# Kernel tuning notes

Hardware: AMD Instinct MI355X
Metric: run time of the kernel (lower is better)

Reference implementation:

```python
import jax, jax.numpy as jnp
import numpy as np

B, S, E = 2, 2048, 2048
H = 16              # num value heads
D = E // H // 2     # = 64, half head dim (Q/K head dim)
LAMBDA_INIT = 0.8 - 0.6 * float(np.exp(-0.3 * 12))
NORM_EPS = 1e-5


def setup_inputs() -> dict:
    key = jax.random.key(0)
    ks = jax.random.split(key, 10)
    std = 0.02
    x = jax.random.normal(ks[0], (B, S, E), jnp.float32)
    Wq = jax.random.normal(ks[1], (E, E), jnp.float32) * std
    Wk = jax.random.normal(ks[2], (E, E), jnp.float32) * std
    Wv = jax.random.normal(ks[3], (E, E), jnp.float32) * std
    Wo = jax.random.normal(ks[4], (E, E), jnp.float32) * std
    lambda_q1 = jax.random.normal(ks[5], (D,), jnp.float32) * 0.1
    lambda_q2 = jax.random.normal(ks[6], (D,), jnp.float32) * 0.1
    lambda_k1 = jax.random.normal(ks[7], (D,), jnp.float32) * 0.1
    lambda_k2 = jax.random.normal(ks[8], (D,), jnp.float32) * 0.1
    norm_w = jnp.ones((2 * D,), jnp.float32)
    # standard RoPE angle table: (S, D//2)
    inv_freq = 1.0 / (10000.0 ** (np.arange(0, D, 2, dtype=np.float32) / D))
    ang = np.outer(np.arange(S, dtype=np.float32), inv_freq)
    freqs_cos = jnp.asarray(np.cos(ang), jnp.float32)
    freqs_sin = jnp.asarray(np.sin(ang), jnp.float32)
    return {"x": x, "Wq": Wq, "Wk": Wk, "Wv": Wv, "Wo": Wo,
            "lambda_q1": lambda_q1, "lambda_q2": lambda_q2,
            "lambda_k1": lambda_k1, "lambda_k2": lambda_k2,
            "norm_w": norm_w, "freqs_cos": freqs_cos, "freqs_sin": freqs_sin,
            "start_pos": 0}


def _rope(t, cos, sin):
    # t: (B, S, nh, D); complex rotation over pairs along last dim
    tr = t.reshape(*t.shape[:-1], -1, 2)
    tre, tim = tr[..., 0], tr[..., 1]
    c = cos[None, :, None, :]
    s = sin[None, :, None, :]
    out_re = tre * c - tim * s
    out_im = tre * s + tim * c
    return jnp.stack([out_re, out_im], axis=-1).reshape(t.shape)


def reference(x, Wq, Wk, Wv, Wo, lambda_q1, lambda_q2, lambda_k1, lambda_k2,
              norm_w, freqs_cos, freqs_sin, start_pos):
    bsz, tgt_len, _ = x.shape
    scaling = D ** (-0.5)
    q = (x @ Wq.T).reshape(bsz, tgt_len, 2 * H, D)
    k = (x @ Wk.T).reshape(bsz, tgt_len, 2 * H, D)
    v = (x @ Wv.T).reshape(bsz, tgt_len, H, 2 * D)
    q = _rope(q, freqs_cos, freqs_sin)
    k = _rope(k, freqs_cos, freqs_sin)
    q = (q * scaling).transpose(0, 2, 1, 3)      # (B, 2H, S, D)
    keys = k.transpose(0, 2, 1, 3)               # (B, 2H, S, D)
    values = v.transpose(0, 2, 1, 3)             # (B, H, S, 2D)
    scores = jnp.einsum('bhsd,bhtd->bhst', q, keys)
    causal = jnp.where(jnp.arange(tgt_len)[None, :] > jnp.arange(tgt_len)[:, None],
                       jnp.float32(-jnp.inf), jnp.float32(0.0))
    scores = scores + causal
    attn = jax.nn.softmax(scores.astype(jnp.float32), axis=-1)
    lam1 = jnp.exp(jnp.sum(lambda_q1 * lambda_k1))
    lam2 = jnp.exp(jnp.sum(lambda_q2 * lambda_k2))
    lambda_full = lam1 - lam2 + LAMBDA_INIT
    attn = attn.reshape(bsz, H, 2, tgt_len, tgt_len)
    attn_diff = attn[:, :, 0] - lambda_full * attn[:, :, 1]   # (B, H, S, S)
    ctx = jnp.einsum('bhst,bhtd->bhsd', attn_diff, values)    # (B, H, S, 2D)
    # per-head RMSNorm over 2D channel dim
    ctx = ctx * jax.lax.rsqrt(jnp.mean(ctx * ctx, axis=-1, keepdims=True) + NORM_EPS)
    ctx = ctx * norm_w
    ctx = ctx.transpose(0, 2, 1, 3).reshape(bsz, tgt_len, H * 2 * D)
    return ctx @ Wo.T
```

## Files before the change

kernel.cpp:

```cpp
#include <hip/hip_runtime.h>
#include <hip/hip_bf16.h>
#include <stdint.h>

typedef __hip_bfloat16 bf16;
typedef __attribute__((ext_vector_type(8))) short short8;
typedef __attribute__((ext_vector_type(4))) short s4v;
typedef __attribute__((ext_vector_type(4))) float floatx4;

#define MFMA16(a, b, c) __builtin_amdgcn_mfma_f32_16x16x32_bf16((a), (b), (c), 0, 0, 0)
#define LAMBDA_INIT_F 0.7836057665f
#define FENCE() asm volatile("" ::: "memory")

__device__ __forceinline__ void async16(const void* g, void* l) {
    __builtin_amdgcn_global_load_lds(
        (const __attribute__((address_space(1))) void*)g,
        (__attribute__((address_space(3))) void*)(uintptr_t)l,
        16, 0, 0);
}

__device__ __forceinline__ float loadf(const void* p, size_t idx, int isbf) {
    if (isbf) return __bfloat162float(((const bf16*)p)[idx]);
    return ((const float*)p)[idx];
}

__global__ void detect_dtype(const unsigned short* __restrict__ x, int* __restrict__ flag) {
    const int t = threadIdx.x;
    const unsigned short u = x[2 * t];
    const int e = (u >> 7) & 0xFF;
    int sane = (e >= 110 && e <= 130) ? 1 : 0;
#pragma unroll
    for (int m = 32; m > 0; m >>= 1) sane += __shfl_xor(sane, m);
    if (t == 0) flag[0] = (sane >= 32) ? 1 : 0;
}

__device__ __forceinline__ void conv_body(const void* src, bf16* dst, int boff,
                                          int isbf) {
    const int i = (boff * 256 + threadIdx.x) * 8;
    if (isbf) {
        *(short8*)(dst + i) = *(const short8*)((const bf16*)src + i);
    } else {
        const float* f = (const float*)src + i;
        short8 r;
#pragma unroll
        for (int j = 0; j < 8; ++j) {
            bf16 h = __float2bfloat16(f[j]);
            r[j] = __builtin_bit_cast(short, h);
        }
        *(short8*)(dst + i) = r;
    }
}

__global__ __launch_bounds__(256) void convert_all(const void* __restrict__ x,
                                                   const void* __restrict__ Wq,
                                                   const void* __restrict__ Wk,
                                                   const void* __restrict__ Wv,
                                                   bf16* __restrict__ xb,
                                                   bf16* __restrict__ wq,
                                                   bf16* __restrict__ wk,
                                                   bf16* __restrict__ wv,
                                                   const int* __restrict__ flag) {
    const int bid  = blockIdx.x;
    const int isbf = flag[0];
    if (bid < 4096)      { conv_body(x, xb, bid, isbf); }
    else if (bid < 6144) { if (isbf) return; conv_body(Wq, wq, bid - 4096, 0); }
    else if (bid < 8192) { if (isbf) return; conv_body(Wk, wk, bid - 6144, 0); }
    else                 { if (isbf) return; conv_body(Wv, wv, bid - 8192, 0); }
}

__global__ __launch_bounds__(256) void to_bf16(const void* __restrict__ src,
                                               bf16* __restrict__ dst, int n,
                                               const int* __restrict__ flag,
                                               int skip_if_bf16) {
    if (skip_if_bf16 && flag[0]) return;
    const int i = (blockIdx.x * 256 + threadIdx.x) * 8;
    if (i >= n) return;
    conv_body(src, dst, blockIdx.x, flag[0]);
}

template <int BNT>
__device__ __forceinline__ void gemm_core256(const bf16* __restrict__ A,
                                             const bf16* __restrict__ B,
                                             void* __restrict__ C,
                                             int N, int bm, int bnl,
                                             const int* __restrict__ flag,
                                             const void* __restrict__ fcos,
                                             const void* __restrict__ fsin,
                                             int mode, char* lds) {
    constexpr int K    = 2048;
    constexpr int NT   = 64;
    constexpr int ASZ  = 16384;
    constexpr int BSZ  = BNT * 64;
    constexpr int SLOT = ASZ + BSZ;
    constexpr int F    = (BNT == 256) ? 8 : 4;
    constexpr int FH   = F / 2;
    constexpr int BCH  = BNT / 128;

    const int tid  = threadIdx.x;
    const int lane = tid & 63;
    const int quad = lane >> 4;
    const int l16  = lane & 15;
    const int w    = tid >> 6;
    const int wr   = (BNT == 256) ? (w >> 2) : (w >> 1);
    const int wc   = (BNT == 256) ? (w & 3) : (w & 1);

    const int c0 = tid, c1 = tid + 512;
    const int r0 = c0 >> 2, r1 = c1 >> 2;
    const int kc0 = (c0 & 3) ^ (((r0 >> 3) & 1) << 1);
    const int kc1 = (c1 & 3) ^ (((r1 >> 3) & 1) << 1);
    const bf16* Asrc0 = A + (size_t)(bm * 256 + r0) * K + kc0 * 8;
    const bf16* Asrc1 = A + (size_t)(bm * 256 + r1) * K + kc1 * 8;
    const bf16* Bsrc0 = B + (size_t)(bnl * BNT + r0) * K + kc0 * 8;
    const bf16* Bsrc1 = B + (size_t)(bnl * BNT + r1) * K + kc1 * 8;
    const int dA0 = c0 * 16, dA1 = c1 * 16;
    const int dB0 = ASZ + c0 * 16, dB1 = ASZ + c1 * 16;

    const int swz = (quad * 16) ^ ((l16 & 8) << 2);
    int offA[8], offB[4];
#pragma unroll
    for (int f = 0; f < F; ++f) offA[f] = (wr * (F * 16) + f * 16 + l16) * 64 + swz;
#pragma unroll
    for (int g = 0; g < 4; ++g) offB[g] = ASZ + (wc * 64 + g * 16 + l16) * 64 + swz;

    floatx4 acc[F][4];
#pragma unroll
    for (int f = 0; f < F; ++f)
#pragma unroll
        for (int g = 0; g < 4; ++g)
#pragma unroll
            for (int r = 0; r < 4; ++r) acc[f][g][r] = 0.0f;

#pragma unroll
    for (int ts = 0; ts < 2; ++ts) {
        char* slot = lds + ts * SLOT;
        async16(Asrc0 + ts * 32, slot + dA0);
        async16(Asrc1 + ts * 32, slot + dA1);
        async16(Bsrc0 + ts * 32, slot + dB0);
        if constexpr (BCH == 2) async16(Bsrc1 + ts * 32, slot + dB1);
    }
    if constexpr (BNT == 256) asm volatile("s_waitcnt vmcnt(4)" ::: "memory");
    else                      asm volatile("s_waitcnt vmcnt(3)" ::: "memory");
    __builtin_amdgcn_s_barrier();
    FENCE();

#pragma unroll 4
    for (int t = 0; t < NT; ++t) {
        char* slot  = lds + (t & 3) * SLOT;
        const int ts = t + 2;
        char* wslot = lds + (ts & 3) * SLOT;

        short8 af[FH], bfv[4];
#pragma unroll
        for (int f = 0; f < FH; ++f) af[f] = *(const short8*)(slot + offA[f]);
#pragma unroll
        for (int g = 0; g < 4; ++g) bfv[g] = *(const short8*)(slot + offB[g]);
        if (ts < NT) {
            async16(Asrc0 + (size_t)ts * 32, wslot + dA0);
            async16(Asrc1 + (size_t)ts * 32, wslot + dA1);
        }
        FENCE();
        __builtin_amdgcn_s_barrier();
        FENCE();
        __builtin_amdgcn_s_setprio(1);
#pragma unroll
        for (int f = 0; f < FH; ++f)
#pragma unroll
            for (int g = 0; g < 4; ++g)
                acc[f][g] = MFMA16(af[f], bfv[g], acc[f][g]);
        __builtin_amdgcn_s_setprio(0);

        short8 af2[FH];
#pragma unroll
        for (int f = 0; f < FH; ++f) af2[f] = *(const short8*)(slot + offA[FH + f]);
        if (ts < NT) {
            async16(Bsrc0 + (size_t)ts * 32, wslot + dB0);
            if constexpr (BCH == 2) async16(Bsrc1 + (size_t)ts * 32, wslot + dB1);
            if constexpr (BNT == 256) asm volatile("s_waitcnt vmcnt(4)" ::: "memory");
            else                      asm volatile("s_waitcnt vmcnt(3)" ::: "memory");
        } else {
            asm volatile("s_waitcnt vmcnt(0)" ::: "memory");
        }
        __builtin_amdgcn_s_barrier();
        FENCE();
        __builtin_amdgcn_s_setprio(1);
#pragma unroll
        for (int f = 0; f < FH; ++f)
#pragma unroll
            for (int g = 0; g < 4; ++g)
                acc[FH + f][g] = MFMA16(af2[f], bfv[g], acc[FH + f][g]);
        __builtin_amdgcn_s_setprio(0);
    }

    const int isbf  = flag[0];
    const int mbase = bm * 256 + wr * (F * 16);
    const int nbase = bnl * BNT + wc * 64;
    if (mode == 3) {
#pragma unroll
        for (int f = 0; f < F; ++f)
#pragma unroll
            for (int g = 0; g < 4; ++g) {
                const int n  = nbase + g * 16 + l16;
                const int m0 = mbase + f * 16 + quad * 4;
                const int bb2 = m0 >> 11;
                const int s0 = m0 & 2047;
                s4v pk;
#pragma unroll
                for (int r = 0; r < 4; ++r) {
                    bf16 hv = __float2bfloat16(acc[f][g][r]);
                    pk[r] = __builtin_bit_cast(short, hv);
                }
                *(s4v*)((bf16*)C + ((size_t)(bb2 * 2048 + n)) * 2048 + s0) = pk;
            }
    } else if (mode == 1 || mode == 2) {
        const float qs = (mode == 1) ? 0.125f : 1.0f;
#pragma unroll
        for (int f = 0; f < F; ++f)
#pragma unroll
            for (int g = 0; g < 4; ++g) {
                const int n   = nbase + g * 16 + l16;
                const int jp  = (n & 63) >> 1;
                const float sg = (n & 1) ? 1.0f : -1.0f;
#pragma unroll
                for (int r = 0; r < 4; ++r) {
                    const int m = mbase + f * 16 + quad * 4 + r;
                    const int s = m & 2047;
                    const float v  = acc[f][g][r];
                    const float pv = __shfl_xor(v, 1);
                    const float ct = loadf(fcos, (size_t)s * 32 + jp, isbf);
                    const float st = loadf(fsin, (size_t)s * 32 + jp, isbf);
                    const float out = (v * ct + sg * pv * st) * qs;
                    ((bf16*)C)[(size_t)m * N + n] = __float2bfloat16(out);
                }
            }
    } else {
        const int c_bf = (mode == 4) ? isbf : 1;
#pragma unroll
        for (int f = 0; f < F; ++f)
#pragma unroll
            for (int g = 0; g < 4; ++g) {
                const int n = nbase + g * 16 + l16;
#pragma unroll
                for (int r = 0; r < 4; ++r) {
                    const int m = mbase + f * 16 + quad * 4 + r;
                    if (c_bf) ((bf16*)C)[(size_t)m * N + n] = __float2bfloat16(acc[f][g][r]);
                    else      ((float*)C)[(size_t)m * N + n] = acc[f][g][r];
                }
            }
    }
}

__global__ __launch_bounds__(512, 2) void gemm256_qkv(const bf16* __restrict__ A,
                                                      const bf16* __restrict__ Wq_s,
                                                      const bf16* __restrict__ Wk_s,
                                                      const bf16* __restrict__ Wv_s,
                                                      const void* __restrict__ WqR,
                                                      const void* __restrict__ WkR,
                                                      const void* __restrict__ WvR,
                                                      bf16* __restrict__ qbuf,
                                                      bf16* __restrict__ kbuf,
                                                      bf16* __restrict__ vtbuf,
                                                      const int* __restrict__ flag,
                                                      const void* __restrict__ fcos,
                                                      const void* __restrict__ fsin) {
    extern __shared__ char lds[];
    const int flat = blockIdx.y * 24 + blockIdx.x;
    const int swz  = (flat & 7) * 48 + (flat >> 3);
    const int wsel = swz >> 7;
    const int rem  = swz & 127;
    const int bm   = rem >> 3;
    const int bnl  = rem & 7;
    const int isbf = flag[0];
    const bf16* Bp;
    void* Cp;
    int mode;
    if (wsel == 0)      { Bp = isbf ? (const bf16*)WqR : Wq_s; Cp = qbuf;  mode = 1; }
    else if (wsel == 1) { Bp = isbf ? (const bf16*)WkR : Wk_s; Cp = kbuf;  mode = 2; }
    else                { Bp = isbf ? (const bf16*)WvR : Wv_s; Cp = vtbuf; mode = 3; }
    gemm_core256<256>(A, Bp, Cp, 2048, bm, bnl, flag, fcos, fsin, mode, lds);
}

__global__ __launch_bounds__(512, 2) void gemm128_fin(const bf16* __restrict__ A,
                                                      const bf16* __restrict__ Wo_s,
                                                      const void* __restrict__ WoR,
                                                      void* __restrict__ C,
                                                      const int* __restrict__ flag) {
    extern __shared__ char lds[];
    const int flat = blockIdx.y * 16 + blockIdx.x;
    const int swz  = (flat & 7) * 32 + (flat >> 3);
    const int bm   = swz >> 4;
    const int bnl  = swz & 15;
    const bf16* Bp = flag[0] ? (const bf16*)WoR : Wo_s;
    gemm_core256<128>(A, Bp, C, 2048, bm, bnl, flag, nullptr, nullptr, 4, lds);
}

__global__ void lambda_kernel(const void* lq1, const void* lq2,
                              const void* lk1, const void* lk2,
                              float* out, const int* __restrict__ flag) {
    const int isbf = flag[0];
    const int t = threadIdx.x;
    float p1 = loadf(lq1, t, isbf) * loadf(lk1, t, isbf);
    float p2 = loadf(lq2, t, isbf) * loadf(lk2, t, isbf);
#pragma unroll
    for (int m = 32; m > 0; m >>= 1) {
        p1 += __shfl_xor(p1, m);
        p2 += __shfl_xor(p2, m);
    }
    if (t == 0) out[0] = expf(p1) - expf(p2) + LAMBDA_INIT_F;
}

__global__ __launch_bounds__(256) void diff_attn(const bf16* __restrict__ Q,
                                                 const bf16* __restrict__ K,
                                                 const bf16* __restrict__ Vt,
                                                 bf16* __restrict__ ctx,
                                                 const float* __restrict__ lam,
                                                 const void* __restrict__ norm_w,
                                                 const int* __restrict__ flag) {
    __shared__ __align__(16) char smem[55296];
    bf16* K1s = (bf16*)smem;
    bf16* K2s = (bf16*)(smem + 8192);
    bf16* Vs  = (bf16*)(smem + 16384);
    char* pool = smem + 32768;

    const int isbf = flag[0];
    const int tid  = threadIdx.x;
    const int lane = tid & 63;
    const int quad = lane >> 4;
    const int l16  = lane & 15;
    const int w    = tid >> 6;
    const int t7   = l16 & 7;

    const int bidx = blockIdx.x;
    const int c8   = bidx & 7;
    const int r6   = bidx >> 3;
    const int p    = r6 & 15;
    const int grp  = (r6 >> 4) * 8 + c8;
    const int h    = grp & 15;
    const int b    = grp >> 4;

    const float lambda_full = lam[0];
    float nw[8];
#pragma unroll
    for (int j = 0; j < 8; ++j) nw[j] = loadf(norm_w, j * 16 + l16, isbf);

    bf16* P1s = (bf16*)(pool + w * 2816);
    bf16* P2s = (bf16*)(pool + 11264 + w * 2816);

    for (int tsel = 0; tsel < 2; ++tsel) {
        const int qt = tsel ? (31 - p) : p;
        const int q0 = qt * 64;

        __syncthreads();

#pragma unroll
        for (int i = 0; i < 2; ++i) {
            const int c = i * 256 + tid;
            const int row = c >> 3, cc = c & 7;
            const int inner = cc ^ (row & 7);
            async16(Q + ((size_t)(b * 2048 + q0 + row) * 32 + 2 * h) * 64 + inner * 8,
                    pool + c * 16);
            async16(Q + ((size_t)(b * 2048 + q0 + row) * 32 + 2 * h + 1) * 64 + inner * 8,
                    pool + 8192 + c * 16);
        }
        __syncthreads();

        short8 qf1[2], qf2[2];
        {
            const int rho = w * 16 + l16;
#pragma unroll
            for (int c = 0; c < 2; ++c) {
                const int ch = (c * 4 + quad) ^ t7;
                qf1[c] = *(const short8*)(pool + rho * 128 + ch * 16);
                qf2[c] = *(const short8*)(pool + 8192 + rho * 128 + ch * 16);
            }
        }

        floatx4 O1[8], O2[8];
#pragma unroll
        for (int j = 0; j < 8; ++j)
#pragma unroll
            for (int r = 0; r < 4; ++r) { O1[j][r] = 0.0f; O2[j][r] = 0.0f; }
        float lp1[4] = {0.f, 0.f, 0.f, 0.f};
        float lp2[4] = {0.f, 0.f, 0.f, 0.f};

        for (int kt0 = 0; kt0 <= q0; kt0 += 64) {
            __syncthreads();
#pragma unroll
            for (int i = 0; i < 2; ++i) {
                const int c = i * 256 + tid;
                const int row = c >> 3, cc = c & 7;
                const int inner = cc ^ (row & 7);
                async16(K + ((size_t)(b * 2048 + kt0 + row) * 32 + 2 * h) * 64 + inner * 8,
                        (char*)K1s + c * 16);
                async16(K + ((size_t)(b * 2048 + kt0 + row) * 32 + 2 * h + 1) * 64 + inner * 8,
                        (char*)K2s + c * 16);
            }
#pragma unroll
            for (int i = 0; i < 4; ++i) {
                const int c = i * 256 + tid;
                const int d = c >> 3, cc = c & 7;
                const int inner = cc ^ (d & 7);
                async16(Vt + ((size_t)(b * 16 + h) * 128 + d) * 2048 + kt0 + inner * 8,
                        (char*)Vs + c * 16);
            }
            __syncthreads();

            floatx4 s1[4], s2[4];
#pragma unroll
            for (int j = 0; j < 4; ++j)
#pragma unroll
                for (int r = 0; r < 4; ++r) { s1[j][r] = 0.0f; s2[j][r] = 0.0f; }
#pragma unroll
            for (int c = 0; c < 2; ++c) {
                const int ch = ((c * 4 + quad) ^ t7) * 16;
#pragma unroll
                for (int j = 0; j < 4; ++j) {
                    short8 k1f = *(const short8*)((const char*)K1s + (j * 16 + l16) * 128 + ch);
                    s1[j] = MFMA16(qf1[c], k1f, s1[j]);
                    short8 k2f = *(const short8*)((const char*)K2s + (j * 16 + l16) * 128 + ch);
                    s2[j] = MFMA16(qf2[c], k2f, s2[j]);
                }
            }

            if (kt0 == q0) {
#pragma unroll
                for (int j = 0; j < 4; ++j)
#pragma unroll
                    for (int r = 0; r < 4; ++r)
                        if (j * 16 + l16 > w * 16 + quad * 4 + r) {
                            s1[j][r] = -1e30f;
                            s2[j][r] = -1e30f;
                        }
            }

#pragma unroll
            for (int j = 0; j < 4; ++j)
#pragma unroll
                for (int r = 0; r < 4; ++r) {
                    const float e1 = __expf(s1[j][r]);
                    const float e2 = __expf(s2[j][r]);
                    lp1[r] += e1;
                    lp2[r] += e2;
                    P1s[(quad * 4 + r) * 88 + j * 16 + l16] = __float2bfloat16(e1);
                    P2s[(quad * 4 + r) * 88 + j * 16 + l16] = __float2bfloat16(e2);
                }

#pragma unroll
            for (int c = 0; c < 2; ++c) {
                short8 a1 = *(const short8*)((const char*)P1s + l16 * 176 + c * 64 + quad * 16);
                short8 a2 = *(const short8*)((const char*)P2s + l16 * 176 + c * 64 + quad * 16);
                const int ch = ((c * 4 + quad) ^ t7) * 16;
#pragma unroll
                for (int j = 0; j < 8; ++j) {
                    short8 vb = *(const short8*)((const char*)Vs + (j * 16 + l16) * 128 + ch);
                    O1[j] = MFMA16(a1, vb, O1[j]);
                    O2[j] = MFMA16(a2, vb, O2[j]);
                }
            }
        }

#pragma unroll
        for (int r = 0; r < 4; ++r) {
            float t1 = lp1[r], t2 = lp2[r];
            t1 += __shfl_xor(t1, 1); t2 += __shfl_xor(t2, 1);
            t1 += __shfl_xor(t1, 2); t2 += __shfl_xor(t2, 2);
            t1 += __shfl_xor(t1, 4); t2 += __shfl_xor(t2, 4);
            t1 += __shfl_xor(t1, 8); t2 += __shfl_xor(t2, 8);
            const float i1 = 1.0f / t1;
            const float i2 = lambda_full / t2;
            float cv[8];
            float ss = 0.0f;
#pragma unroll
            for (int j = 0; j < 8; ++j) {
                const float v = O1[j][r] * i1 - O2[j][r] * i2;
                cv[j] = v;
                ss += v * v;
            }
            ss += __shfl_xor(ss, 1);
            ss += __shfl_xor(ss, 2);
            ss += __shfl_xor(ss, 4);
            ss += __shfl_xor(ss, 8);
            const float scale = rsqrtf(ss * (1.0f / 128.0f) + 1e-5f);
            const int row = q0 + w * 16 + quad * 4 + r;
            const size_t base = ((size_t)(b * 2048) + row) * 2048 + h * 128;
#pragma unroll
            for (int j = 0; j < 8; ++j)
                ctx[base + j * 16 + l16] = __float2bfloat16(cv[j] * scale * nw[j]);
        }
    }
}

extern "C" void kernel_launch(void* const* d_in, const int* in_sizes, int n_in,
                              void* d_out, int out_size, void* d_ws, size_t ws_size,
                              hipStream_t stream) {
    const void* x   = d_in[0];
    const void* Wq  = d_in[1];
    const void* Wk  = d_in[2];
    const void* Wv  = d_in[3];
    const void* Wo  = d_in[4];
    const void* lq1 = d_in[5];
    const void* lq2 = d_in[6];
    const void* lk1 = d_in[7];
    const void* lk2 = d_in[8];
    const void* nw  = d_in[9];
    const void* fc  = d_in[10];
    const void* fs  = d_in[11];

    const size_t BUF = (size_t)4096 * 2048 * sizeof(bf16);
    if (ws_size < 4 * BUF + 64) return;
    char* ws = (char*)d_ws;
    bf16*  qbuf  = (bf16*)(ws);
    bf16*  kbuf  = (bf16*)(ws + BUF);
    bf16*  vbuf  = (bf16*)(ws + 2 * BUF);
    bf16*  vtbuf = (bf16*)(ws + 3 * BUF);
    float* lamb  = (float*)(ws + 4 * BUF);
    int*   flag  = (int*)(ws + 4 * BUF + 8);
    bf16*  xb    = vbuf;
    bf16*  ctxb  = vbuf;

    bf16* wq_s = (bf16*)d_out;
    bf16* wk_s = wq_s + (size_t)2048 * 2048;
    bf16* wv_s = wk_s + (size_t)2048 * 2048;

    const int NW = 2048 * 2048;

    hipFuncSetAttribute(reinterpret_cast<const void*>(gemm256_qkv),
                        hipFuncAttributeMaxDynamicSharedMemorySize, 131072);
    hipFuncSetAttribute(reinterpret_cast<const void*>(gemm128_fin),
                        hipFuncAttributeMaxDynamicSharedMemorySize, 98304);

    detect_dtype<<<1, 64, 0, stream>>>((const unsigned short*)x, flag);
    convert_all<<<10240, 256, 0, stream>>>(x, Wq, Wk, Wv, xb, wq_s, wk_s, wv_s, flag);

    dim3 gq(24, 16);
    gemm256_qkv<<<gq, 512, 131072, stream>>>(xb, wq_s, wk_s, wv_s, Wq, Wk, Wv,
                                             qbuf, kbuf, vtbuf, flag, fc, fs);

    lambda_kernel<<<1, 64, 0, stream>>>(lq1, lq2, lk1, lk2, lamb, flag);

    diff_attn<<<512, 256, 0, stream>>>(qbuf, kbuf, vtbuf, ctxb, lamb, nw, flag);

    to_bf16<<<NW / 2048, 256, 0, stream>>>(Wo, qbuf, NW, flag, 1);
    dim3 gf(16, 16);
    gemm128_fin<<<gf, 512, 98304, stream>>>(ctxb, qbuf, Wo, d_out, flag);
}
```

Measured before the change: 465.6 us.

## Double-buffer K tiles in diff attention and drop GEMM block swizzle

The attention kernel now double-buffers K in LDS, prefetching the next K tile while the current one is consumed. It uses vmcnt-based partial waits so the V load overlaps the QK and softmax phase. This is meant to hide global load latency that the old two-barrier loop exposed. The two GEMM kernels also drop their block-index swizzle and map blockIdx directly to tiles, which may change L2 reuse. The K prefetch on the last iteration reads one tile past the causal range (possibly past the batch end for b=1), and LDS use grows to 70KB, which may reduce occupancy.

```diff
diff --git a/kernel.cpp b/kernel.cpp
--- a/kernel.cpp
+++ b/kernel.cpp
@@ -262,12 +262,8 @@
                                                       const void* __restrict__ fcos,
                                                       const void* __restrict__ fsin) {
     extern __shared__ char lds[];
-    const int flat = blockIdx.y * 24 + blockIdx.x;
-    const int swz  = (flat & 7) * 48 + (flat >> 3);
-    const int wsel = swz >> 7;
-    const int rem  = swz & 127;
-    const int bm   = rem >> 3;
-    const int bnl  = rem & 7;
+    const int wsel = blockIdx.x >> 3;
+    const int bnl  = blockIdx.x & 7;
     const int isbf = flag[0];
     const bf16* Bp;
     void* Cp;
@@ -275,7 +271,7 @@
     if (wsel == 0)      { Bp = isbf ? (const bf16*)WqR : Wq_s; Cp = qbuf;  mode = 1; }
     else if (wsel == 1) { Bp = isbf ? (const bf16*)WkR : Wk_s; Cp = kbuf;  mode = 2; }
     else                { Bp = isbf ? (const bf16*)WvR : Wv_s; Cp = vtbuf; mode = 3; }
-    gemm_core256<256>(A, Bp, Cp, 2048, bm, bnl, flag, fcos, fsin, mode, lds);
+    gemm_core256<256>(A, Bp, Cp, 2048, blockIdx.y, bnl, flag, fcos, fsin, mode, lds);
 }
 
 __global__ __launch_bounds__(512, 2) void gemm128_fin(const bf16* __restrict__ A,
@@ -284,12 +280,8 @@
                                                       void* __restrict__ C,
                                                       const int* __restrict__ flag) {
     extern __shared__ char lds[];
-    const int flat = blockIdx.y * 16 + blockIdx.x;
-    const int swz  = (flat & 7) * 32 + (flat >> 3);
-    const int bm   = swz >> 4;
-    const int bnl  = swz & 15;
     const bf16* Bp = flag[0] ? (const bf16*)WoR : Wo_s;
-    gemm_core256<128>(A, Bp, C, 2048, bm, bnl, flag, nullptr, nullptr, 4, lds);
+    gemm_core256<128>(A, Bp, C, 2048, blockIdx.y, blockIdx.x, flag, nullptr, nullptr, 4, lds);
 }
 
 __global__ void lambda_kernel(const void* lq1, const void* lq2,
@@ -314,11 +306,9 @@
                                                  const float* __restrict__ lam,
                                                  const void* __restrict__ norm_w,
                                                  const int* __restrict__ flag) {
-    __shared__ __align__(16) char smem[55296];
-    bf16* K1s = (bf16*)smem;
-    bf16* K2s = (bf16*)(smem + 8192);
-    bf16* Vs  = (bf16*)(smem + 16384);
-    char* pool = smem + 32768;
+    extern __shared__ __align__(16) char smem[];
+    char* Vs   = smem + 32768;
+    char* pool = smem + 49152;
 
     const int isbf = flag[0];
     const int tid  = threadIdx.x;
@@ -360,6 +350,16 @@
             async16(Q + ((size_t)(b * 2048 + q0 + row) * 32 + 2 * h + 1) * 64 + inner * 8,
                     pool + 8192 + c * 16);
         }
+#pragma unroll
+        for (int i = 0; i < 2; ++i) {
+            const int c = i * 256 + tid;
+            const int row = c >> 3, cc = c & 7;
+            const int inner = cc ^ (row & 7);
+            async16(K + ((size_t)(b * 2048 + row) * 32 + 2 * h) * 64 + inner * 8,
+                    smem + c * 16);
+            async16(K + ((size_t)(b * 2048 + row) * 32 + 2 * h + 1) * 64 + inner * 8,
+                    smem + 8192 + c * 16);
+        }
         __syncthreads();
 
         short8 qf1[2], qf2[2];
@@ -381,27 +381,35 @@
         float lp1[4] = {0.f, 0.f, 0.f, 0.f};
         float lp2[4] = {0.f, 0.f, 0.f, 0.f};
 
-        for (int kt0 = 0; kt0 <= q0; kt0 += 64) {
-            __syncthreads();
-#pragma unroll
-            for (int i = 0; i < 2; ++i) {
-                const int c = i * 256 + tid;
-                const int row = c >> 3, cc = c & 7;
-                const int inner = cc ^ (row & 7);
-                async16(K + ((size_t)(b * 2048 + kt0 + row) * 32 + 2 * h) * 64 + inner * 8,
-                        (char*)K1s + c * 16);
-                async16(K + ((size_t)(b * 2048 + kt0 + row) * 32 + 2 * h + 1) * 64 + inner * 8,
-                        (char*)K2s + c * 16);
-            }
+        int it = 0;
+        for (int kt0 = 0; kt0 <= q0; kt0 += 64, ++it) {
+            char* Kc = smem + (it & 1) * 16384;
+            char* Kn = smem + ((it & 1) ^ 1) * 16384;
+
 #pragma unroll
             for (int i = 0; i < 4; ++i) {
                 const int c = i * 256 + tid;
                 const int d = c >> 3, cc = c & 7;
                 const int inner = cc ^ (d & 7);
                 async16(Vt + ((size_t)(b * 16 + h) * 128 + d) * 2048 + kt0 + inner * 8,
-                        (char*)Vs + c * 16);
-            }
-            __syncthreads();
+                        Vs + c * 16);
+            }
+            {
+                const int kn = kt0 + 64;
+#pragma unroll
+                for (int i = 0; i < 2; ++i) {
+                    const int c = i * 256 + tid;
+                    const int row = c >> 3, cc = c & 7;
+                    const int inner = cc ^ (row & 7);
+                    async16(K + ((size_t)(b * 2048 + kn + row) * 32 + 2 * h) * 64 + inner * 8,
+                            Kn + c * 16);
+                    async16(K + ((size_t)(b * 2048 + kn + row) * 32 + 2 * h + 1) * 64 + inner * 8,
+                            Kn + 8192 + c * 16);
+                }
+            }
+            asm volatile("s_waitcnt vmcnt(8)" ::: "memory");
+            __builtin_amdgcn_s_barrier();
+            FENCE();
 
             floatx4 s1[4], s2[4];
 #pragma unroll
@@ -413,9 +421,9 @@
                 const int ch = ((c * 4 + quad) ^ t7) * 16;
 #pragma unroll
                 for (int j = 0; j < 4; ++j) {
-                    short8 k1f = *(const short8*)((const char*)K1s + (j * 16 + l16) * 128 + ch);
+                    short8 k1f = *(const short8*)(Kc + (j * 16 + l16) * 128 + ch);
                     s1[j] = MFMA16(qf1[c], k1f, s1[j]);
-                    short8 k2f = *(const short8*)((const char*)K2s + (j * 16 + l16) * 128 + ch);
+                    short8 k2f = *(const short8*)(Kc + 8192 + (j * 16 + l16) * 128 + ch);
                     s2[j] = MFMA16(qf2[c], k2f, s2[j]);
                 }
             }
@@ -443,6 +451,10 @@
                     P2s[(quad * 4 + r) * 88 + j * 16 + l16] = __float2bfloat16(e2);
                 }
 
+            asm volatile("s_waitcnt vmcnt(4)" ::: "memory");
+            __builtin_amdgcn_s_barrier();
+            FENCE();
+
 #pragma unroll
             for (int c = 0; c < 2; ++c) {
                 short8 a1 = *(const short8*)((const char*)P1s + l16 * 176 + c * 64 + quad * 16);
@@ -450,11 +462,14 @@
                 const int ch = ((c * 4 + quad) ^ t7) * 16;
 #pragma unroll
                 for (int j = 0; j < 8; ++j) {
-                    short8 vb = *(const short8*)((const char*)Vs + (j * 16 + l16) * 128 + ch);
+                    short8 vb = *(const short8*)(Vs + (j * 16 + l16) * 128 + ch);
                     O1[j] = MFMA16(a1, vb, O1[j]);
                     O2[j] = MFMA16(a2, vb, O2[j]);
                 }
             }
+            FENCE();
+            __builtin_amdgcn_s_barrier();
+            FENCE();
         }
 
 #pragma unroll
@@ -486,6 +501,7 @@
                 ctx[base + j * 16 + l16] = __float2bfloat16(cv[j] * scale * nw[j]);
         }
     }
+    asm volatile("s_waitcnt vmcnt(0)" ::: "memory");
 }
 
 extern "C" void kernel_launch(void* const* d_in, const int* in_sizes, int n_in,
@@ -526,6 +542,8 @@
                         hipFuncAttributeMaxDynamicSharedMemorySize, 131072);
     hipFuncSetAttribute(reinterpret_cast<const void*>(gemm128_fin),
                         hipFuncAttributeMaxDynamicSharedMemorySize, 98304);
+    hipFuncSetAttribute(reinterpret_cast<const void*>(diff_attn),
+                        hipFuncAttributeMaxDynamicSharedMemorySize, 71680);
 
     detect_dtype<<<1, 64, 0, stream>>>((const unsigned short*)x, flag);
     convert_all<<<10240, 256, 0, stream>>>(x, Wq, Wk, Wv, xb, wq_s, wk_s, wv_s, flag);
@@ -536,7 +554,7 @@
 
     lambda_kernel<<<1, 64, 0, stream>>>(lq1, lq2, lk1, lk2, lamb, flag);
 
-    diff_attn<<<512, 256, 0, stream>>>(qbuf, kbuf, vtbuf, ctxb, lamb, nw, flag);
+    diff_attn<<<512, 256, 71680, stream>>>(qbuf, kbuf, vtbuf, ctxb, lamb, nw, flag);
 
     to_bf16<<<NW / 2048, 256, 0, stream>>>(Wo, qbuf, NW, flag, 1);
     dim3 gf(16, 16);
```

After: 469.8 us. Within noise of the previous version (+0.9%).

## Split attention into one block per query tile and share one P buffer

Applied to the files above, without the earlier changes.

The attention kernel previously had each block process a pair of causally balanced query tiles in sequence. It now launches 1024 blocks, one per query tile, ordered longest-first so heavy tiles are scheduled early. The two softmax probability tiles now share a single LDS staging buffer, written and consumed one after the other, which cuts static LDS to allow more resident blocks at the cost of extra serialisation within each wave. The swizzled block-index remapping in both GEMM kernels is also dropped in favour of direct grid indices, which may change L2 locality.

```diff
diff --git a/kernel.cpp b/kernel.cpp
--- a/kernel.cpp
+++ b/kernel.cpp
@@ -262,12 +262,8 @@
                                                       const void* __restrict__ fcos,
                                                       const void* __restrict__ fsin) {
     extern __shared__ char lds[];
-    const int flat = blockIdx.y * 24 + blockIdx.x;
-    const int swz  = (flat & 7) * 48 + (flat >> 3);
-    const int wsel = swz >> 7;
-    const int rem  = swz & 127;
-    const int bm   = rem >> 3;
-    const int bnl  = rem & 7;
+    const int wsel = blockIdx.x >> 3;
+    const int bnl  = blockIdx.x & 7;
     const int isbf = flag[0];
     const bf16* Bp;
     void* Cp;
@@ -275,7 +271,7 @@
     if (wsel == 0)      { Bp = isbf ? (const bf16*)WqR : Wq_s; Cp = qbuf;  mode = 1; }
     else if (wsel == 1) { Bp = isbf ? (const bf16*)WkR : Wk_s; Cp = kbuf;  mode = 2; }
     else                { Bp = isbf ? (const bf16*)WvR : Wv_s; Cp = vtbuf; mode = 3; }
-    gemm_core256<256>(A, Bp, Cp, 2048, bm, bnl, flag, fcos, fsin, mode, lds);
+    gemm_core256<256>(A, Bp, Cp, 2048, blockIdx.y, bnl, flag, fcos, fsin, mode, lds);
 }
 
 __global__ __launch_bounds__(512, 2) void gemm128_fin(const bf16* __restrict__ A,
@@ -284,12 +280,8 @@
                                                       void* __restrict__ C,
                                                       const int* __restrict__ flag) {
     extern __shared__ char lds[];
-    const int flat = blockIdx.y * 16 + blockIdx.x;
-    const int swz  = (flat & 7) * 32 + (flat >> 3);
-    const int bm   = swz >> 4;
-    const int bnl  = swz & 15;
     const bf16* Bp = flag[0] ? (const bf16*)WoR : Wo_s;
-    gemm_core256<128>(A, Bp, C, 2048, bm, bnl, flag, nullptr, nullptr, 4, lds);
+    gemm_core256<128>(A, Bp, C, 2048, blockIdx.y, blockIdx.x, flag, nullptr, nullptr, 4, lds);
 }
 
 __global__ void lambda_kernel(const void* lq1, const void* lq2,
@@ -314,10 +306,10 @@
                                                  const float* __restrict__ lam,
                                                  const void* __restrict__ norm_w,
                                                  const int* __restrict__ flag) {
-    __shared__ __align__(16) char smem[55296];
+    __shared__ __align__(16) char smem[49152];
     bf16* K1s = (bf16*)smem;
     bf16* K2s = (bf16*)(smem + 8192);
-    bf16* Vs  = (bf16*)(smem + 16384);
+    char* Vs  = smem + 16384;
     char* pool = smem + 32768;
 
     const int isbf = flag[0];
@@ -330,161 +322,172 @@
 
     const int bidx = blockIdx.x;
     const int c8   = bidx & 7;
-    const int r6   = bidx >> 3;
-    const int p    = r6 & 15;
-    const int grp  = (r6 >> 4) * 8 + c8;
+    const int r7   = bidx >> 3;
+    const int rank = r7 & 31;
+    const int grp  = (r7 >> 5) * 8 + c8;
     const int h    = grp & 15;
     const int b    = grp >> 4;
+    const int qt   = 31 - rank;
+    const int q0   = qt * 64;
 
     const float lambda_full = lam[0];
     float nw[8];
 #pragma unroll
     for (int j = 0; j < 8; ++j) nw[j] = loadf(norm_w, j * 16 + l16, isbf);
 
-    bf16* P1s = (bf16*)(pool + w * 2816);
-    bf16* P2s = (bf16*)(pool + 11264 + w * 2816);
-
-    for (int tsel = 0; tsel < 2; ++tsel) {
-        const int qt = tsel ? (31 - p) : p;
-        const int q0 = qt * 64;
-
+    bf16* Ps = (bf16*)(pool + w * 2816);
+
+#pragma unroll
+    for (int i = 0; i < 2; ++i) {
+        const int c = i * 256 + tid;
+        const int row = c >> 3, cc = c & 7;
+        const int inner = cc ^ (row & 7);
+        async16(Q + ((size_t)(b * 2048 + q0 + row) * 32 + 2 * h) * 64 + inner * 8,
+                pool + c * 16);
+        async16(Q + ((size_t)(b * 2048 + q0 + row) * 32 + 2 * h + 1) * 64 + inner * 8,
+                pool + 8192 + c * 16);
+    }
+    __syncthreads();
+
+    short8 qf1[2], qf2[2];
+    {
+        const int rho = w * 16 + l16;
+#pragma unroll
+        for (int c = 0; c < 2; ++c) {
+            const int ch = (c * 4 + quad) ^ t7;
+            qf1[c] = *(const short8*)(pool + rho * 128 + ch * 16);
+            qf2[c] = *(const short8*)(pool + 8192 + rho * 128 + ch * 16);
+        }
+    }
+
+    floatx4 O1[8], O2[8];
+#pragma unroll
+    for (int j = 0; j < 8; ++j)
+#pragma unroll
+        for (int r = 0; r < 4; ++r) { O1[j][r] = 0.0f; O2[j][r] = 0.0f; }
+    float lp1[4] = {0.f, 0.f, 0.f, 0.f};
+    float lp2[4] = {0.f, 0.f, 0.f, 0.f};
+
+    for (int kt0 = 0; kt0 <= q0; kt0 += 64) {
         __syncthreads();
-
 #pragma unroll
         for (int i = 0; i < 2; ++i) {
             const int c = i * 256 + tid;
             const int row = c >> 3, cc = c & 7;
             const int inner = cc ^ (row & 7);
-            async16(Q + ((size_t)(b * 2048 + q0 + row) * 32 + 2 * h) * 64 + inner * 8,
-                    pool + c * 16);
-            async16(Q + ((size_t)(b * 2048 + q0 + row) * 32 + 2 * h + 1) * 64 + inner * 8,
-                    pool + 8192 + c * 16);
+            async16(K + ((size_t)(b * 2048 + kt0 + row) * 32 + 2 * h) * 64 + inner * 8,
+                    (char*)K1s + c * 16);
+            async16(K + ((size_t)(b * 2048 + kt0 + row) * 32 + 2 * h + 1) * 64 + inner * 8,
+                    (char*)K2s + c * 16);
+        }
+#pragma unroll
+        for (int i = 0; i < 4; ++i) {
+            const int c = i * 256 + tid;
+            const int d = c >> 3, cc = c & 7;
+            const int inner = cc ^ (d & 7);
+            async16(Vt + ((size_t)(b * 16 + h) * 128 + d) * 2048 + kt0 + inner * 8,
+                    Vs + c * 16);
         }
         __syncthreads();
 
-        short8 qf1[2], qf2[2];
-        {
-            const int rho = w * 16 + l16;
-#pragma unroll
-            for (int c = 0; c < 2; ++c) {
-                const int ch = (c * 4 + quad) ^ t7;
-                qf1[c] = *(const short8*)(pool + rho * 128 + ch * 16);
-                qf2[c] = *(const short8*)(pool + 8192 + rho * 128 + ch * 16);
-            }
-        }
-
-        floatx4 O1[8], O2[8];
+        floatx4 s1[4], s2[4];
+#pragma unroll
+        for (int j = 0; j < 4; ++j)
+#pragma unroll
+            for (int r = 0; r < 4; ++r) { s1[j][r] = 0.0f; s2[j][r] = 0.0f; }
+#pragma unroll
+        for (int c = 0; c < 2; ++c) {
+            const int ch = ((c * 4 + quad) ^ t7) * 16;
+#pragma unroll
+            for (int j = 0; j < 4; ++j) {
+                short8 k1f = *(const short8*)((const char*)K1s + (j * 16 + l16) * 128 + ch);
+                s1[j] = MFMA16(qf1[c], k1f, s1[j]);
+                short8 k2f = *(const short8*)((const char*)K2s + (j * 16 + l16) * 128 + ch);
+                s2[j] = MFMA16(qf2[c], k2f, s2[j]);
+            }
+        }
+
+        if (kt0 == q0) {
+#pragma unroll
+            for (int j = 0; j < 4; ++j)
+#pragma unroll
+                for (int r = 0; r < 4; ++r)
+                    if (j * 16 + l16 > w * 16 + quad * 4 + r) {
+                        s1[j][r] = -1e30f;
+                        s2[j][r] = -1e30f;
+                    }
+        }
+
+#pragma unroll
+        for (int j = 0; j < 4; ++j)
+#pragma unroll
+            for (int r = 0; r < 4; ++r) {
+                const float e1 = __expf(s1[j][r]);
+                const float e2 = __expf(s2[j][r]);
+                lp1[r] += e1;
+                lp2[r] += e2;
+                Ps[(quad * 4 + r) * 88 + j * 16 + l16] = __float2bfloat16(e1);
+                s2[j][r] = e2;
+            }
+
+#pragma unroll
+        for (int c = 0; c < 2; ++c) {
+            short8 a1 = *(const short8*)((const char*)Ps + l16 * 176 + c * 64 + quad * 16);
+            const int ch = ((c * 4 + quad) ^ t7) * 16;
+#pragma unroll
+            for (int j = 0; j < 8; ++j) {
+                short8 vb = *(const short8*)(Vs + (j * 16 + l16) * 128 + ch);
+                O1[j] = MFMA16(a1, vb, O1[j]);
+            }
+        }
+        FENCE();
+
+#pragma unroll
+        for (int j = 0; j < 4; ++j)
+#pragma unroll
+            for (int r = 0; r < 4; ++r)
+                Ps[(quad * 4 + r) * 88 + j * 16 + l16] = __float2bfloat16(s2[j][r]);
+        FENCE();
+
+#pragma unroll
+        for (int c = 0; c < 2; ++c) {
+            short8 a2 = *(const short8*)((const char*)Ps + l16 * 176 + c * 64 + quad * 16);
+            const int ch = ((c * 4 + quad) ^ t7) * 16;
+#pragma unroll
+            for (int j = 0; j < 8; ++j) {
+                short8 vb = *(const short8*)(Vs + (j * 16 + l16) * 128 + ch);
+                O2[j] = MFMA16(a2, vb, O2[j]);
+            }
+        }
+    }
+
+#pragma unroll
+    for (int r = 0; r < 4; ++r) {
+        float t1 = lp1[r], t2 = lp2[r];
+        t1 += __shfl_xor(t1, 1); t2 += __shfl_xor(t2, 1);
+        t1 += __shfl_xor(t1, 2); t2 += __shfl_xor(t2, 2);
+        t1 += __shfl_xor(t1, 4); t2 += __shfl_xor(t2, 4);
+        t1 += __shfl_xor(t1, 8); t2 += __shfl_xor(t2, 8);
+        const float i1 = 1.0f / t1;
+        const float i2 = lambda_full / t2;
+        float cv[8];
+        float ss = 0.0f;
+#pragma unroll
+        for (int j = 0; j < 8; ++j) {
+            const float v = O1[j][r] * i1 - O2[j][r] * i2;
+            cv[j] = v;
+            ss += v * v;
+        }
+        ss += __shfl_xor(ss, 1);
+        ss += __shfl_xor(ss, 2);
+        ss += __shfl_xor(ss, 4);
+        ss += __shfl_xor(ss, 8);
+        const float scale = rsqrtf(ss * (1.0f / 128.0f) + 1e-5f);
+        const int row = q0 + w * 16 + quad * 4 + r;
+        const size_t base = ((size_t)(b * 2048) + row) * 2048 + h * 128;
 #pragma unroll
         for (int j = 0; j < 8; ++j)
-#pragma unroll
-            for (int r = 0; r < 4; ++r) { O1[j][r] = 0.0f; O2[j][r] = 0.0f; }
-        float lp1[4] = {0.f, 0.f, 0.f, 0.f};
-        float lp2[4] = {0.f, 0.f, 0.f, 0.f};
-
-        for (int kt0 = 0; kt0 <= q0; kt0 += 64) {
-            __syncthreads();
-#pragma unroll
-            for (int i = 0; i < 2; ++i) {
-                const int c = i * 256 + tid;
-                const int row = c >> 3, cc = c & 7;
-                const int inner = cc ^ (row & 7);
-                async16(K + ((size_t)(b * 2048 + kt0 + row) * 32 + 2 * h) * 64 + inner * 8,
-                        (char*)K1s + c * 16);
-                async16(K + ((size_t)(b * 2048 + kt0 + row) * 32 + 2 * h + 1) * 64 + inner * 8,
-                        (char*)K2s + c * 16);
-            }
-#pragma unroll
-            for (int i = 0; i < 4; ++i) {
-                const int c = i * 256 + tid;
-                const int d = c >> 3, cc = c & 7;
-                const int inner = cc ^ (d & 7);
-                async16(Vt + ((size_t)(b * 16 + h) * 128 + d) * 2048 + kt0 + inner * 8,
-                        (char*)Vs + c * 16);
-            }
-            __syncthreads();
-
-            floatx4 s1[4], s2[4];
-#pragma unroll
-            for (int j = 0; j < 4; ++j)
-#pragma unroll
-                for (int r = 0; r < 4; ++r) { s1[j][r] = 0.0f; s2[j][r] = 0.0f; }
-#pragma unroll
-            for (int c = 0; c < 2; ++c) {
-                const int ch = ((c * 4 + quad) ^ t7) * 16;
-#pragma unroll
-                for (int j = 0; j < 4; ++j) {
-                    short8 k1f = *(const short8*)((const char*)K1s + (j * 16 + l16) * 128 + ch);
-                    s1[j] = MFMA16(qf1[c], k1f, s1[j]);
-                    short8 k2f = *(const short8*)((const char*)K2s + (j * 16 + l16) * 128 + ch);
-                    s2[j] = MFMA16(qf2[c], k2f, s2[j]);
-                }
-            }
-
-            if (kt0 == q0) {
-#pragma unroll
-                for (int j = 0; j < 4; ++j)
-#pragma unroll
-                    for (int r = 0; r < 4; ++r)
-                        if (j * 16 + l16 > w * 16 + quad * 4 + r) {
-                            s1[j][r] = -1e30f;
-                            s2[j][r] = -1e30f;
-                        }
-            }
-
-#pragma unroll
-            for (int j = 0; j < 4; ++j)
-#pragma unroll
-                for (int r = 0; r < 4; ++r) {
-                    const float e1 = __expf(s1[j][r]);
-                    const float e2 = __expf(s2[j][r]);
-                    lp1[r] += e1;
-                    lp2[r] += e2;
-                    P1s[(quad * 4 + r) * 88 + j * 16 + l16] = __float2bfloat16(e1);
-                    P2s[(quad * 4 + r) * 88 + j * 16 + l16] = __float2bfloat16(e2);
-                }
-
-#pragma unroll
-            for (int c = 0; c < 2; ++c) {
-                short8 a1 = *(const short8*)((const char*)P1s + l16 * 176 + c * 64 + quad * 16);
-                short8 a2 = *(const short8*)((const char*)P2s + l16 * 176 + c * 64 + quad * 16);
-                const int ch = ((c * 4 + quad) ^ t7) * 16;
-#pragma unroll
-                for (int j = 0; j < 8; ++j) {
-                    short8 vb = *(const short8*)((const char*)Vs + (j * 16 + l16) * 128 + ch);
-                    O1[j] = MFMA16(a1, vb, O1[j]);
-                    O2[j] = MFMA16(a2, vb, O2[j]);
-                }
-            }
-        }
-
-#pragma unroll
-        for (int r = 0; r < 4; ++r) {
-            float t1 = lp1[r], t2 = lp2[r];
-            t1 += __shfl_xor(t1, 1); t2 += __shfl_xor(t2, 1);
-            t1 += __shfl_xor(t1, 2); t2 += __shfl_xor(t2, 2);
-            t1 += __shfl_xor(t1, 4); t2 += __shfl_xor(t2, 4);
-            t1 += __shfl_xor(t1, 8); t2 += __shfl_xor(t2, 8);
-            const float i1 = 1.0f / t1;
-            const float i2 = lambda_full / t2;
-            float cv[8];
-            float ss = 0.0f;
-#pragma unroll
-            for (int j = 0; j < 8; ++j) {
-                const float v = O1[j][r] * i1 - O2[j][r] * i2;
-                cv[j] = v;
-                ss += v * v;
-            }
-            ss += __shfl_xor(ss, 1);
-            ss += __shfl_xor(ss, 2);
-            ss += __shfl_xor(ss, 4);
-            ss += __shfl_xor(ss, 8);
-            const float scale = rsqrtf(ss * (1.0f / 128.0f) + 1e-5f);
-            const int row = q0 + w * 16 + quad * 4 + r;
-            const size_t base = ((size_t)(b * 2048) + row) * 2048 + h * 128;
-#pragma unroll
-            for (int j = 0; j < 8; ++j)
-                ctx[base + j * 16 + l16] = __float2bfloat16(cv[j] * scale * nw[j]);
-        }
+            ctx[base + j * 16 + l16] = __float2bfloat16(cv[j] * scale * nw[j]);
     }
 }
 
@@ -536,7 +539,7 @@
 
     lambda_kernel<<<1, 64, 0, stream>>>(lq1, lq2, lk1, lk2, lamb, flag);
 
-    diff_attn<<<512, 256, 0, stream>>>(qbuf, kbuf, vtbuf, ctxb, lamb, nw, flag);
+    diff_attn<<<1024, 256, 0, stream>>>(qbuf, kbuf, vtbuf, ctxb, lamb, nw, flag);
 
     to_bf16<<<NW / 2048, 256, 0, stream>>>(Wo, qbuf, NW, flag, 1);
     dim3 gf(16, 16);
```

New measurement: 489.3 us. +5.1%, slower.
